# Kernel tuning notes

Hardware: AMD Instinct MI355X
Metric: run time of the kernel (lower is better)

Reference implementation:

```python
import jax, jax.numpy as jnp
import numpy as np

B, T, E = 8, 2048, 512  # batch, seq_len, dim (single head, head_dim == dim)
EPS = 1e-3


def setup_inputs() -> dict:
    key = jax.random.key(0)
    ks = jax.random.split(key, 6)
    s = E ** -0.5  # scale proj weights like nn.Linear init so exp(k) stays finite
    return {
        "x": jax.random.normal(ks[0], (B, E, T), jnp.float32),
        "toep_weight": jax.random.normal(ks[1], (1, T), jnp.float32),
        "q_w": jax.random.normal(ks[2], (E, E), jnp.float32) * s,
        "q_b": jnp.zeros((E,), jnp.float32),
        "k_w": jax.random.normal(ks[3], (E, E), jnp.float32) * s,
        "k_b": jnp.zeros((E,), jnp.float32),
        "v_w": jax.random.normal(ks[4], (E, E), jnp.float32) * s,
        "v_b": jnp.zeros((E,), jnp.float32),
        "o_w": jax.random.normal(ks[5], (E, E), jnp.float32) * s,
        "o_b": jnp.zeros((E,), jnp.float32),
    }


def reference(x, toep_weight, q_w, q_b, k_w, k_b, v_w, v_b, o_w, o_b):
    # x: (B, E, T) -> (B, T, E)
    xt = jnp.transpose(x, (0, 2, 1))
    q = xt @ q_w.T + q_b
    k = xt @ k_w.T + k_b
    v = xt @ v_w.T + v_b
    # feature maps: softmax(q) * d^-1/2 , exp(k); v scaled by per-position Toeplitz weight
    q = jax.nn.softmax(q, axis=-1) * (E ** -0.5)
    k = jnp.exp(k)
    v = v * toep_weight[0][:, None]  # (T,1) broadcast over (B,T,E)
    # causal linear attention: running outer-product state S (B,E,E) and key-sum z (B,E)
    qs = jnp.transpose(q, (1, 0, 2))  # (T, B, E)
    kk = jnp.transpose(k, (1, 0, 2))
    vv = jnp.transpose(v, (1, 0, 2))

    def step(carry, inp):
        S, z = carry
        qt, kt, vt = inp  # each (B, E)
        S = S + kt[:, :, None] * vt[:, None, :]  # cumulative k v^T
        z = z + kt                                # cumulative key sum
        d = jnp.maximum(jnp.sum(z * qt, axis=-1), EPS)  # clamp then reciprocal
        out = jnp.einsum('bd,bde->be', qt, S) / d[:, None]
        return (S, z), out

    S0 = jnp.zeros((B, E, E), q.dtype)
    z0 = jnp.zeros((B, E), q.dtype)
    _, outs = jax.lax.scan(step, (S0, z0), (qs, kk, vv))  # outs: (T, B, E)
    attn = jnp.transpose(outs, (1, 0, 2))  # (B, T, E)
    return attn @ o_w.T + o_b
```

## Files before the change

### kernel.cpp

```cpp
#include <hip/hip_runtime.h>
#include <hip/hip_bf16.h>
#include <math.h>
#include <stdint.h>

#define B_ 8
#define T_ 2048
#define E_ 512
#define CCH 256
#define NC_ 8
#define EPS_ 1e-3f
#define QSCALE 0.044194173824159216f

typedef __attribute__((ext_vector_type(8))) short short8;
typedef __attribute__((ext_vector_type(4))) float f32x4;
typedef __hip_bfloat16 bf16_t;

__device__ __forceinline__ short f2bs(float x) {
    bf16_t h = __float2bfloat16(x);
    return __builtin_bit_cast(short, h);
}

__device__ __forceinline__ void async16(const void* g, void* l) {
    __builtin_amdgcn_global_load_lds(
        (const __attribute__((address_space(1))) unsigned int*)(unsigned long long)(uintptr_t)g,
        (__attribute__((address_space(3))) unsigned int*)(unsigned int)(uintptr_t)l,
        16, 0, 0);
}

__device__ __forceinline__ void gemm128(const short* __restrict__ Ag, int lda,
                                        const short* __restrict__ Bg, int ldb, int K,
                                        short* Al, short* Bl, f32x4 acc[4][4],
                                        int wm, int wn, int wq, int lane) {
    int m16 = lane & 15, quad = lane >> 4;
    for (int k0 = 0; k0 < K; k0 += 32) {
        __syncthreads();
        #pragma unroll
        for (int cc = 0; cc < 2; ++cc) {
            int row = wq * 32 + cc * 16 + (lane >> 2);
            int kc = (lane & 3) * 8;
            async16(Ag + (size_t)row * lda + k0 + kc, Al + (wq * 32 + cc * 16) * 32);
            async16(Bg + (size_t)row * ldb + k0 + kc, Bl + (wq * 32 + cc * 16) * 32);
        }
        __syncthreads();
        short8 a[4], b[4];
        #pragma unroll
        for (int i = 0; i < 4; ++i)
            a[i] = *(const short8*)(Al + (wm + i * 16 + m16) * 32 + quad * 8);
        #pragma unroll
        for (int i = 0; i < 4; ++i)
            b[i] = *(const short8*)(Bl + (wn + i * 16 + m16) * 32 + quad * 8);
        #pragma unroll
        for (int i = 0; i < 4; ++i)
            #pragma unroll
            for (int j = 0; j < 4; ++j)
                acc[i][j] = __builtin_amdgcn_mfma_f32_16x16x32_bf16(a[i], b[j], acc[i][j], 0, 0, 0);
    }
}

#define GEMM_PROLOG \
    int tid = threadIdx.x, lane = tid & 63, wq = tid >> 6; \
    int wm = (wq & 1) * 64, wn = (wq >> 1) * 64; \
    int m16 = lane & 15, quad = lane >> 4; \
    (void)tid; \
    f32x4 acc[4][4]; \
    { f32x4 zz = {0.f, 0.f, 0.f, 0.f}; \
      for (int i = 0; i < 4; ++i) for (int j = 0; j < 4; ++j) acc[i][j] = zz; }

__global__ void castw_kernel(const float* __restrict__ qw, const float* __restrict__ kw,
                             const float* __restrict__ vw, const float* __restrict__ ow,
                             short* __restrict__ wbf) {
    size_t idx8 = ((size_t)blockIdx.x * 256 + threadIdx.x) * 8;
    int sel = (int)(idx8 >> 18);
    size_t off = idx8 & ((1u << 18) - 1);
    const float* src = sel == 0 ? qw : sel == 1 ? kw : sel == 2 ? vw : ow;
    const float4* sp = (const float4*)(src + off);
    float4 a = sp[0], b = sp[1];
    short8 g;
    g[0] = f2bs(a.x); g[1] = f2bs(a.y); g[2] = f2bs(a.z); g[3] = f2bs(a.w);
    g[4] = f2bs(b.x); g[5] = f2bs(b.y); g[6] = f2bs(b.z); g[7] = f2bs(b.w);
    *(short8*)(wbf + idx8) = g;
}

__global__ void transpose_x_kernel(const float* __restrict__ x, short* __restrict__ xbf) {
    __shared__ __align__(16) float S[64][68];
    int tid = threadIdx.x;
    int t0 = blockIdx.x * 64, e0 = blockIdx.y * 64, b = blockIdx.z;
    const float* src = x + ((size_t)b * E_ + e0) * T_ + t0;
    short* dst = xbf + ((size_t)b * T_ + t0) * E_ + e0;
    #pragma unroll
    for (int p = 0; p < 2; ++p) {
        int el = p * 32 + (tid >> 3), tc = (tid & 7) * 8;
        const float4* sp = (const float4*)(src + (size_t)el * T_ + tc);
        *(float4*)&S[el][tc] = sp[0];
        *(float4*)&S[el][tc + 4] = sp[1];
    }
    __syncthreads();
    #pragma unroll
    for (int p = 0; p < 2; ++p) {
        int tl = p * 32 + (tid >> 3), ec = (tid & 7) * 8;
        short8 g;
        #pragma unroll
        for (int j = 0; j < 8; ++j) g[j] = f2bs(S[ec + j][tl]);
        *(short8*)(dst + (size_t)tl * E_ + ec) = g;
    }
}

__global__ void transpose_bf_kernel(const short* __restrict__ k, const short* __restrict__ v,
                                    short* __restrict__ kT, short* __restrict__ vT) {
    __shared__ __align__(16) short S[64][72];
    int tid = threadIdx.x;
    int t0 = blockIdx.x * 64, e0 = blockIdx.y * 64;
    int b = blockIdx.z >> 1, which = blockIdx.z & 1;
    const short* src = (which ? v : k) + ((size_t)b * T_ + t0) * E_ + e0;
    short* dst = (which ? vT : kT) + ((size_t)b * E_ + e0) * T_ + t0;
    #pragma unroll
    for (int p = 0; p < 2; ++p) {
        int tl = p * 32 + (tid >> 3), ec = (tid & 7) * 8;
        *(short8*)&S[tl][ec] = *(const short8*)(src + (size_t)tl * E_ + ec);
    }
    __syncthreads();
    #pragma unroll
    for (int p = 0; p < 2; ++p) {
        int er = p * 32 + (tid >> 3), tc = (tid & 7) * 8;
        short8 g;
        #pragma unroll
        for (int j = 0; j < 8; ++j) g[j] = S[tc + j][er];
        *(short8*)(dst + (size_t)er * T_ + tc) = g;
    }
}

__global__ __launch_bounds__(256) void proj_qkv_kernel(
    const short* __restrict__ xbf, const short* __restrict__ wbf,
    const float* __restrict__ qb, const float* __restrict__ kb, const float* __restrict__ vb,
    const float* __restrict__ toep,
    float* __restrict__ qf, bf16_t* __restrict__ kout, bf16_t* __restrict__ vout) {
    __shared__ __align__(16) short Al[128 * 32], Bl[128 * 32];
    GEMM_PROLOG
    int t0 = blockIdx.x * 128, i0 = blockIdx.y * 128;
    int b = blockIdx.z / 3, sel = blockIdx.z % 3;
    const short* Ag = xbf + ((size_t)b * T_ + t0) * E_;
    const short* Bg = wbf + (size_t)sel * E_ * E_ + (size_t)i0 * E_;
    gemm128(Ag, E_, Bg, E_, E_, Al, Bl, acc, wm, wn, wq, lane);
    const float* bias = (sel == 0) ? qb : (sel == 1) ? kb : vb;
    #pragma unroll
    for (int mt = 0; mt < 4; ++mt)
        #pragma unroll
        for (int r = 0; r < 4; ++r) {
            int t = t0 + wm + mt * 16 + quad * 4 + r;
            size_t rowoff = ((size_t)b * T_ + t) * E_;
            float tw = toep[t];
            #pragma unroll
            for (int nt = 0; nt < 4; ++nt) {
                int col = i0 + wn + nt * 16 + m16;
                float vv = acc[mt][nt][r] + bias[col];
                if (sel == 0) qf[rowoff + col] = vv;
                else if (sel == 1) kout[rowoff + col] = __float2bfloat16(expf(vv));
                else vout[rowoff + col] = __float2bfloat16(vv * tw);
            }
        }
}

__global__ void softmax_kernel(const float* __restrict__ qf, bf16_t* __restrict__ qbf) {
    __shared__ float red[256];
    int row = blockIdx.x, tid = threadIdx.x;
    const float* p = qf + (size_t)row * E_;
    float v0 = p[tid], v1 = p[tid + 256];
    red[tid] = fmaxf(v0, v1);
    __syncthreads();
    for (int s = 128; s > 0; s >>= 1) { if (tid < s) red[tid] = fmaxf(red[tid], red[tid + s]); __syncthreads(); }
    float m = red[0];
    __syncthreads();
    float e0 = expf(v0 - m), e1 = expf(v1 - m);
    red[tid] = e0 + e1;
    __syncthreads();
    for (int s = 128; s > 0; s >>= 1) { if (tid < s) red[tid] += red[tid + s]; __syncthreads(); }
    float inv = QSCALE / red[0];
    qbf[(size_t)row * E_ + tid] = __float2bfloat16(e0 * inv);
    qbf[(size_t)row * E_ + tid + 256] = __float2bfloat16(e1 * inv);
}

__global__ __launch_bounds__(256) void chunk_kv_kernel(
    const short* __restrict__ vT, const short* __restrict__ kT, bf16_t* __restrict__ KV) {
    __shared__ __align__(16) short Al[128 * 32], Bl[128 * 32];
    GEMM_PROLOG
    int ev0 = blockIdx.x * 128, ek0 = blockIdx.y * 128;
    int bc = blockIdx.z, b = bc >> 3, c = bc & 7;
    const short* Ag = vT + ((size_t)b * E_ + ev0) * T_ + c * CCH;
    const short* Bg = kT + ((size_t)b * E_ + ek0) * T_ + c * CCH;
    gemm128(Ag, T_, Bg, T_, CCH, Al, Bl, acc, wm, wn, wq, lane);
    #pragma unroll
    for (int mt = 0; mt < 4; ++mt)
        #pragma unroll
        for (int r = 0; r < 4; ++r) {
            int ev = ev0 + wm + mt * 16 + quad * 4 + r;
            #pragma unroll
            for (int nt = 0; nt < 4; ++nt) {
                int ek = ek0 + wn + nt * 16 + m16;
                KV[((size_t)bc * E_ + ev) * E_ + ek] = __float2bfloat16(acc[mt][nt][r]);
            }
        }
}

__global__ void scan_kv_kernel(bf16_t* __restrict__ KV) {
    size_t gid = (size_t)blockIdx.x * 256 + threadIdx.x;
    size_t b = gid >> 18, idx = gid & ((1u << 18) - 1);
    bf16_t* p = KV + b * ((size_t)NC_ * E_ * E_) + idx;
    float run = 0.f;
    for (int c = 0; c < NC_; ++c) {
        float t = __bfloat162float(*p);
        *p = __float2bfloat16(run);
        run += t;
        p += (size_t)E_ * E_;
    }
}

__global__ void ksum_kernel(const bf16_t* __restrict__ k, float* __restrict__ ks) {
    int bc = blockIdx.x, b = bc >> 3, c = bc & 7;
    int e = blockIdx.y * 256 + threadIdx.x;
    const bf16_t* kp = k + ((size_t)b * T_ + (size_t)c * CCH) * E_ + e;
    float s = 0.f;
    for (int t = 0; t < CCH; ++t) s += __bfloat162float(kp[(size_t)t * E_]);
    ks[(size_t)bc * E_ + e] = s;
}
__global__ void scan_f_kernel(float* __restrict__ buf, int nper) {
    int gid = blockIdx.x * 256 + threadIdx.x;
    int b = gid / nper, idx = gid % nper;
    float run = 0.f;
    float* p = buf + (size_t)b * NC_ * nper + idx;
    for (int c = 0; c < NC_; ++c) { float t = *p; *p = run; run += t; p += nper; }
}

__global__ __launch_bounds__(256) void pmat_kernel(
    const short* __restrict__ qbf, const short* __restrict__ kbf, bf16_t* __restrict__ P) {
    __shared__ __align__(16) short Al[128 * 32], Bl[128 * 32];
    int tj0 = blockIdx.x * 128, ti0 = blockIdx.y * 128;
    int bc = blockIdx.z, b = bc >> 3, c = bc & 7;
    short* Pp = (short*)P + (size_t)bc * CCH * CCH;
    if (tj0 > ti0) {
        short8 z8 = {0, 0, 0, 0, 0, 0, 0, 0};
        for (int i = threadIdx.x; i < 128 * 128 / 8; i += 256) {
            int row = i >> 4, colc = (i * 8) & 127;
            *(short8*)(Pp + (size_t)(ti0 + row) * CCH + tj0 + colc) = z8;
        }
        return;
    }
    GEMM_PROLOG
    const short* Ag = qbf + ((size_t)b * T_ + c * CCH + ti0) * E_;
    const short* Bg = kbf + ((size_t)b * T_ + c * CCH + tj0) * E_;
    gemm128(Ag, E_, Bg, E_, E_, Al, Bl, acc, wm, wn, wq, lane);
    #pragma unroll
    for (int mt = 0; mt < 4; ++mt)
        #pragma unroll
        for (int r = 0; r < 4; ++r) {
            int row = ti0 + wm + mt * 16 + quad * 4 + r;
            #pragma unroll
            for (int nt = 0; nt < 4; ++nt) {
                int col = tj0 + wn + nt * 16 + m16;
                float vv = (col <= row) ? acc[mt][nt][r] : 0.f;
                ((bf16_t*)Pp)[(size_t)row * CCH + col] = __float2bfloat16(vv);
            }
        }
}

__global__ void denom_kernel(const bf16_t* __restrict__ qbf, const float* __restrict__ z,
                             const bf16_t* __restrict__ P, float* __restrict__ invd) {
    __shared__ float red[256];
    int row = blockIdx.x, tid = threadIdx.x;
    int b = row >> 11, t = row & (T_ - 1);
    int c = t >> 8, tl = t & 255;
    const bf16_t* qr = qbf + (size_t)row * E_;
    const float* zr = z + ((size_t)(b * NC_ + c)) * E_;
    const bf16_t* Pr = P + (((size_t)(b * NC_ + c)) * CCH + tl) * CCH;
    float s = __bfloat162float(qr[tid]) * zr[tid]
            + __bfloat162float(qr[tid + 256]) * zr[tid + 256]
            + __bfloat162float(Pr[tid]);
    red[tid] = s;
    __syncthreads();
    for (int st = 128; st > 0; st >>= 1) { if (tid < st) red[tid] += red[tid + st]; __syncthreads(); }
    if (tid == 0) invd[row] = 1.f / fmaxf(red[0], EPS_);
}

__global__ __launch_bounds__(256) void attnout_kernel(
    const short* __restrict__ qbf, const short* __restrict__ KV,
    const short* __restrict__ P, const short* __restrict__ vT,
    const float* __restrict__ invd, bf16_t* __restrict__ attn) {
    __shared__ __align__(16) short Al[128 * 32], Bl[128 * 32];
    GEMM_PROLOG
    int t0 = blockIdx.x * 128, i0 = blockIdx.y * 128, b = blockIdx.z;
    int c = t0 >> 8, tl0 = t0 & 255, bc = b * NC_ + c;
    gemm128(qbf + ((size_t)b * T_ + t0) * E_, E_,
            KV + ((size_t)bc * E_ + i0) * E_, E_, E_, Al, Bl, acc, wm, wn, wq, lane);
    gemm128(P + ((size_t)bc * CCH + tl0) * CCH, CCH,
            vT + ((size_t)b * E_ + i0) * T_ + c * CCH, T_, CCH, Al, Bl, acc, wm, wn, wq, lane);
    #pragma unroll
    for (int mt = 0; mt < 4; ++mt)
        #pragma unroll
        for (int r = 0; r < 4; ++r) {
            int t = t0 + wm + mt * 16 + quad * 4 + r;
            float sc = invd[(size_t)b * T_ + t];
            #pragma unroll
            for (int nt = 0; nt < 4; ++nt) {
                int col = i0 + wn + nt * 16 + m16;
                attn[((size_t)b * T_ + t) * E_ + col] = __float2bfloat16(acc[mt][nt][r] * sc);
            }
        }
}

__global__ __launch_bounds__(256) void outproj_kernel(
    const short* __restrict__ attn, const short* __restrict__ wbf_o,
    const float* __restrict__ ob, float* __restrict__ out) {
    __shared__ __align__(16) short Al[128 * 32], Bl[128 * 32];
    GEMM_PROLOG
    int t0 = blockIdx.x * 128, i0 = blockIdx.y * 128, b = blockIdx.z;
    gemm128(attn + ((size_t)b * T_ + t0) * E_, E_,
            wbf_o + (size_t)i0 * E_, E_, E_, Al, Bl, acc, wm, wn, wq, lane);
    #pragma unroll
    for (int mt = 0; mt < 4; ++mt)
        #pragma unroll
        for (int r = 0; r < 4; ++r) {
            int t = t0 + wm + mt * 16 + quad * 4 + r;
            #pragma unroll
            for (int nt = 0; nt < 4; ++nt) {
                int col = i0 + wn + nt * 16 + m16;
                out[((size_t)b * T_ + t) * E_ + col] = acc[mt][nt][r] + ob[col];
            }
        }
}

extern "C" void kernel_launch(void* const* d_in, const int* in_sizes, int n_in,
                              void* d_out, int out_size, void* d_ws, size_t ws_size,
                              hipStream_t stream) {
    const float* x    = (const float*)d_in[0];
    const float* toep = (const float*)d_in[1];
    const float* q_w  = (const float*)d_in[2];
    const float* q_b  = (const float*)d_in[3];
    const float* k_w  = (const float*)d_in[4];
    const float* k_b  = (const float*)d_in[5];
    const float* v_w  = (const float*)d_in[6];
    const float* v_b  = (const float*)d_in[7];
    const float* o_w  = (const float*)d_in[8];
    const float* o_b  = (const float*)d_in[9];

    const size_t NTE = (size_t)B_ * T_ * E_;
    char* base = (char*)d_ws;
    short* xbf  = (short*)base;  base += NTE * 2;
    short* wbf  = (short*)base;  base += (size_t)4 * E_ * E_ * 2;
    short* qbf  = (short*)base;  base += NTE * 2;
    short* kbf  = (short*)base;  base += NTE * 2;
    short* vbf  = (short*)base;  base += NTE * 2;
    short* kT   = (short*)base;  base += NTE * 2;
    short* vT   = (short*)base;  base += NTE * 2;
    short* KV   = (short*)base;  base += (size_t)B_ * NC_ * E_ * E_ * 2;
    short* P    = (short*)base;  base += (size_t)B_ * NC_ * CCH * CCH * 2;
    float* ksum = (float*)base;  base += (size_t)B_ * NC_ * E_ * 4;
    float* invd = (float*)base;  base += (size_t)B_ * T_ * 4;
    float* qf   = (float*)base;  base += NTE * 4;
    short* attn = xbf;
    float* out  = (float*)d_out;

    dim3 blk(256);
    castw_kernel<<<dim3(512), blk, 0, stream>>>(q_w, k_w, v_w, o_w, wbf);
    transpose_x_kernel<<<dim3(32, 8, 8), blk, 0, stream>>>(x, xbf);
    proj_qkv_kernel<<<dim3(16, 4, 24), blk, 0, stream>>>(
        xbf, wbf, q_b, k_b, v_b, toep, qf, (bf16_t*)kbf, (bf16_t*)vbf);
    softmax_kernel<<<dim3(B_ * T_), blk, 0, stream>>>(qf, (bf16_t*)qbf);
    transpose_bf_kernel<<<dim3(32, 8, 16), blk, 0, stream>>>(kbf, vbf, kT, vT);
    chunk_kv_kernel<<<dim3(4, 4, 64), blk, 0, stream>>>(vT, kT, (bf16_t*)KV);
    scan_kv_kernel<<<dim3(8192), blk, 0, stream>>>((bf16_t*)KV);
    ksum_kernel<<<dim3(64, 2), blk, 0, stream>>>((const bf16_t*)kbf, ksum);
    scan_f_kernel<<<dim3(16), blk, 0, stream>>>(ksum, E_);
    pmat_kernel<<<dim3(2, 2, 64), blk, 0, stream>>>(qbf, kbf, (bf16_t*)P);
    denom_kernel<<<dim3(B_ * T_), blk, 0, stream>>>(
        (const bf16_t*)qbf, ksum, (const bf16_t*)P, invd);
    attnout_kernel<<<dim3(16, 4, 8), blk, 0, stream>>>(
        qbf, KV, P, vT, invd, (bf16_t*)attn);
    outproj_kernel<<<dim3(16, 4, 8), blk, 0, stream>>>(
        attn, wbf + (size_t)3 * E_ * E_, o_b, out);
}
```

Before: 296.4 us.

## Double GEMM K-step to 64 with swizzled LDS layout; store raw q as bf16

The shared GEMM helper now stages 64-wide K tiles per barrier pair instead of 32. The LDS layout is rearranged so each async 16-byte load covers 8 rows by 64 columns, and the MFMA operand reads follow that layout. This halves the number of synchronisations per GEMM at the cost of twice the LDS per block. Separately, the pre-softmax q projection is written as bf16 instead of fp32, which halves that intermediate's traffic but adds rounding error before the softmax.

```diff
diff --git a/kernel.cpp b/kernel.cpp
--- a/kernel.cpp
+++ b/kernel.cpp
@@ -32,28 +32,32 @@
                                         short* Al, short* Bl, f32x4 acc[4][4],
                                         int wm, int wn, int wq, int lane) {
     int m16 = lane & 15, quad = lane >> 4;
-    for (int k0 = 0; k0 < K; k0 += 32) {
+    int r8 = lane & 7, c8 = (lane >> 3) * 8;
+    for (int k0 = 0; k0 < K; k0 += 64) {
         __syncthreads();
         #pragma unroll
-        for (int cc = 0; cc < 2; ++cc) {
-            int row = wq * 32 + cc * 16 + (lane >> 2);
-            int kc = (lane & 3) * 8;
-            async16(Ag + (size_t)row * lda + k0 + kc, Al + (wq * 32 + cc * 16) * 32);
-            async16(Bg + (size_t)row * ldb + k0 + kc, Bl + (wq * 32 + cc * 16) * 32);
+        for (int w = 0; w < 4; ++w) {
+            int R = wq * 32 + w * 8;
+            async16(Ag + (size_t)(R + r8) * lda + k0 + c8, Al + R * 64);
+            async16(Bg + (size_t)(R + r8) * ldb + k0 + c8, Bl + R * 64);
         }
         __syncthreads();
-        short8 a[4], b[4];
-        #pragma unroll
-        for (int i = 0; i < 4; ++i)
-            a[i] = *(const short8*)(Al + (wm + i * 16 + m16) * 32 + quad * 8);
-        #pragma unroll
-        for (int i = 0; i < 4; ++i)
-            b[i] = *(const short8*)(Bl + (wn + i * 16 + m16) * 32 + quad * 8);
-        #pragma unroll
-        for (int i = 0; i < 4; ++i)
-            #pragma unroll
-            for (int j = 0; j < 4; ++j)
-                acc[i][j] = __builtin_amdgcn_mfma_f32_16x16x32_bf16(a[i], b[j], acc[i][j], 0, 0, 0);
+        #pragma unroll
+        for (int h = 0; h < 2; ++h) {
+            int co = (h * 4 + quad) * 64 + (m16 >> 3) * 512 + (m16 & 7) * 8;
+            short8 a[4], b[4];
+            #pragma unroll
+            for (int i = 0; i < 4; ++i)
+                a[i] = *(const short8*)(Al + (wm + i * 16) * 64 + co);
+            #pragma unroll
+            for (int i = 0; i < 4; ++i)
+                b[i] = *(const short8*)(Bl + (wn + i * 16) * 64 + co);
+            #pragma unroll
+            for (int i = 0; i < 4; ++i)
+                #pragma unroll
+                for (int j = 0; j < 4; ++j)
+                    acc[i][j] = __builtin_amdgcn_mfma_f32_16x16x32_bf16(a[i], b[j], acc[i][j], 0, 0, 0);
+        }
     }
 }
 
@@ -133,8 +137,8 @@
     const short* __restrict__ xbf, const short* __restrict__ wbf,
     const float* __restrict__ qb, const float* __restrict__ kb, const float* __restrict__ vb,
     const float* __restrict__ toep,
-    float* __restrict__ qf, bf16_t* __restrict__ kout, bf16_t* __restrict__ vout) {
-    __shared__ __align__(16) short Al[128 * 32], Bl[128 * 32];
+    bf16_t* __restrict__ qraw, bf16_t* __restrict__ kout, bf16_t* __restrict__ vout) {
+    __shared__ __align__(16) short Al[128 * 64], Bl[128 * 64];
     GEMM_PROLOG
     int t0 = blockIdx.x * 128, i0 = blockIdx.y * 128;
     int b = blockIdx.z / 3, sel = blockIdx.z % 3;
@@ -153,18 +157,18 @@
             for (int nt = 0; nt < 4; ++nt) {
                 int col = i0 + wn + nt * 16 + m16;
                 float vv = acc[mt][nt][r] + bias[col];
-                if (sel == 0) qf[rowoff + col] = vv;
+                if (sel == 0) qraw[rowoff + col] = __float2bfloat16(vv);
                 else if (sel == 1) kout[rowoff + col] = __float2bfloat16(expf(vv));
                 else vout[rowoff + col] = __float2bfloat16(vv * tw);
             }
         }
 }
 
-__global__ void softmax_kernel(const float* __restrict__ qf, bf16_t* __restrict__ qbf) {
+__global__ void softmax_kernel(const bf16_t* __restrict__ qraw, bf16_t* __restrict__ qbf) {
     __shared__ float red[256];
     int row = blockIdx.x, tid = threadIdx.x;
-    const float* p = qf + (size_t)row * E_;
-    float v0 = p[tid], v1 = p[tid + 256];
+    const bf16_t* p = qraw + (size_t)row * E_;
+    float v0 = __bfloat162float(p[tid]), v1 = __bfloat162float(p[tid + 256]);
     red[tid] = fmaxf(v0, v1);
     __syncthreads();
     for (int s = 128; s > 0; s >>= 1) { if (tid < s) red[tid] = fmaxf(red[tid], red[tid + s]); __syncthreads(); }
@@ -181,7 +185,7 @@
 
 __global__ __launch_bounds__(256) void chunk_kv_kernel(
     const short* __restrict__ vT, const short* __restrict__ kT, bf16_t* __restrict__ KV) {
-    __shared__ __align__(16) short Al[128 * 32], Bl[128 * 32];
+    __shared__ __align__(16) short Al[128 * 64], Bl[128 * 64];
     GEMM_PROLOG
     int ev0 = blockIdx.x * 128, ek0 = blockIdx.y * 128;
     int bc = blockIdx.z, b = bc >> 3, c = bc & 7;
@@ -232,7 +236,7 @@
 
 __global__ __launch_bounds__(256) void pmat_kernel(
     const short* __restrict__ qbf, const short* __restrict__ kbf, bf16_t* __restrict__ P) {
-    __shared__ __align__(16) short Al[128 * 32], Bl[128 * 32];
+    __shared__ __align__(16) short Al[128 * 64], Bl[128 * 64];
     int tj0 = blockIdx.x * 128, ti0 = blockIdx.y * 128;
     int bc = blockIdx.z, b = bc >> 3, c = bc & 7;
     short* Pp = (short*)P + (size_t)bc * CCH * CCH;
@@ -284,7 +288,7 @@
     const short* __restrict__ qbf, const short* __restrict__ KV,
     const short* __restrict__ P, const short* __restrict__ vT,
     const float* __restrict__ invd, bf16_t* __restrict__ attn) {
-    __shared__ __align__(16) short Al[128 * 32], Bl[128 * 32];
+    __shared__ __align__(16) short Al[128 * 64], Bl[128 * 64];
     GEMM_PROLOG
     int t0 = blockIdx.x * 128, i0 = blockIdx.y * 128, b = blockIdx.z;
     int c = t0 >> 8, tl0 = t0 & 255, bc = b * NC_ + c;
@@ -309,7 +313,7 @@
 __global__ __launch_bounds__(256) void outproj_kernel(
     const short* __restrict__ attn, const short* __restrict__ wbf_o,
     const float* __restrict__ ob, float* __restrict__ out) {
-    __shared__ __align__(16) short Al[128 * 32], Bl[128 * 32];
+    __shared__ __align__(16) short Al[128 * 64], Bl[128 * 64];
     GEMM_PROLOG
     int t0 = blockIdx.x * 128, i0 = blockIdx.y * 128, b = blockIdx.z;
     gemm128(attn + ((size_t)b * T_ + t0) * E_, E_,
@@ -345,6 +349,7 @@
     char* base = (char*)d_ws;
     short* xbf  = (short*)base;  base += NTE * 2;
     short* wbf  = (short*)base;  base += (size_t)4 * E_ * E_ * 2;
+    short* qraw = (short*)base;  base += NTE * 2;
     short* qbf  = (short*)base;  base += NTE * 2;
     short* kbf  = (short*)base;  base += NTE * 2;
     short* vbf  = (short*)base;  base += NTE * 2;
@@ -354,7 +359,6 @@
     short* P    = (short*)base;  base += (size_t)B_ * NC_ * CCH * CCH * 2;
     float* ksum = (float*)base;  base += (size_t)B_ * NC_ * E_ * 4;
     float* invd = (float*)base;  base += (size_t)B_ * T_ * 4;
-    float* qf   = (float*)base;  base += NTE * 4;
     short* attn = xbf;
     float* out  = (float*)d_out;
 
@@ -362,8 +366,8 @@
     castw_kernel<<<dim3(512), blk, 0, stream>>>(q_w, k_w, v_w, o_w, wbf);
     transpose_x_kernel<<<dim3(32, 8, 8), blk, 0, stream>>>(x, xbf);
     proj_qkv_kernel<<<dim3(16, 4, 24), blk, 0, stream>>>(
-        xbf, wbf, q_b, k_b, v_b, toep, qf, (bf16_t*)kbf, (bf16_t*)vbf);
-    softmax_kernel<<<dim3(B_ * T_), blk, 0, stream>>>(qf, (bf16_t*)qbf);
+        xbf, wbf, q_b, k_b, v_b, toep, (bf16_t*)qraw, (bf16_t*)kbf, (bf16_t*)vbf);
+    softmax_kernel<<<dim3(B_ * T_), blk, 0, stream>>>((const bf16_t*)qraw, (bf16_t*)qbf);
     transpose_bf_kernel<<<dim3(32, 8, 16), blk, 0, stream>>>(kbf, vbf, kT, vT);
     chunk_kv_kernel<<<dim3(4, 4, 64), blk, 0, stream>>>(vT, kT, (bf16_t*)KV);
     scan_kv_kernel<<<dim3(8192), blk, 0, stream>>>((bf16_t*)KV);
```

New measurement: 319.8 us. +7.9%, slower.

## Merge independent launches, store q as bf16, and rework LDS layout in GEMM

Applied to the files above, without the earlier changes.

Independent kernels are merged into combined launches that branch on block index: weight cast with x transpose, softmax with key-sum, chunk KV with P matrix, and the two prefix scans. This cuts the kernel count from 12 to 8 and lets small kernels share the GPU with larger ones. The raw q projection is now written as bf16 instead of fp32, halving that intermediate's traffic at the cost of rounding before softmax. The async LDS load layout in gemm128 is changed so each wave fills contiguous 16-row windows and fragments are read with a different stride, likely to reduce bank conflicts.

```diff
diff --git a/kernel.cpp b/kernel.cpp
--- a/kernel.cpp
+++ b/kernel.cpp
@@ -32,23 +32,24 @@
                                         short* Al, short* Bl, f32x4 acc[4][4],
                                         int wm, int wn, int wq, int lane) {
     int m16 = lane & 15, quad = lane >> 4;
+    int r16 = lane & 15, c4 = (lane >> 4) * 8;
     for (int k0 = 0; k0 < K; k0 += 32) {
         __syncthreads();
         #pragma unroll
-        for (int cc = 0; cc < 2; ++cc) {
-            int row = wq * 32 + cc * 16 + (lane >> 2);
-            int kc = (lane & 3) * 8;
-            async16(Ag + (size_t)row * lda + k0 + kc, Al + (wq * 32 + cc * 16) * 32);
-            async16(Bg + (size_t)row * ldb + k0 + kc, Bl + (wq * 32 + cc * 16) * 32);
+        for (int w = 0; w < 2; ++w) {
+            int win = wq + w * 4;
+            int R = win * 16;
+            async16(Ag + (size_t)(R + r16) * lda + k0 + c4, Al + win * 512);
+            async16(Bg + (size_t)(R + r16) * ldb + k0 + c4, Bl + win * 512);
         }
         __syncthreads();
         short8 a[4], b[4];
         #pragma unroll
         for (int i = 0; i < 4; ++i)
-            a[i] = *(const short8*)(Al + (wm + i * 16 + m16) * 32 + quad * 8);
+            a[i] = *(const short8*)(Al + (wm + i * 16) * 32 + quad * 128 + m16 * 8);
         #pragma unroll
         for (int i = 0; i < 4; ++i)
-            b[i] = *(const short8*)(Bl + (wn + i * 16 + m16) * 32 + quad * 8);
+            b[i] = *(const short8*)(Bl + (wn + i * 16) * 32 + quad * 128 + m16 * 8);
         #pragma unroll
         for (int i = 0; i < 4; ++i)
             #pragma unroll
@@ -66,25 +67,28 @@
     { f32x4 zz = {0.f, 0.f, 0.f, 0.f}; \
       for (int i = 0; i < 4; ++i) for (int j = 0; j < 4; ++j) acc[i][j] = zz; }
 
-__global__ void castw_kernel(const float* __restrict__ qw, const float* __restrict__ kw,
-                             const float* __restrict__ vw, const float* __restrict__ ow,
-                             short* __restrict__ wbf) {
-    size_t idx8 = ((size_t)blockIdx.x * 256 + threadIdx.x) * 8;
-    int sel = (int)(idx8 >> 18);
-    size_t off = idx8 & ((1u << 18) - 1);
-    const float* src = sel == 0 ? qw : sel == 1 ? kw : sel == 2 ? vw : ow;
-    const float4* sp = (const float4*)(src + off);
-    float4 a = sp[0], b = sp[1];
-    short8 g;
-    g[0] = f2bs(a.x); g[1] = f2bs(a.y); g[2] = f2bs(a.z); g[3] = f2bs(a.w);
-    g[4] = f2bs(b.x); g[5] = f2bs(b.y); g[6] = f2bs(b.z); g[7] = f2bs(b.w);
-    *(short8*)(wbf + idx8) = g;
-}
-
-__global__ void transpose_x_kernel(const float* __restrict__ x, short* __restrict__ xbf) {
+__global__ void prep_kernel(const float* __restrict__ qw, const float* __restrict__ kw,
+                            const float* __restrict__ vw, const float* __restrict__ ow,
+                            short* __restrict__ wbf,
+                            const float* __restrict__ x, short* __restrict__ xbf) {
+    int bid = blockIdx.x;
+    int tid = threadIdx.x;
+    if (bid < 512) {
+        size_t idx8 = ((size_t)bid * 256 + tid) * 8;
+        int sel = (int)(idx8 >> 18);
+        size_t off = idx8 & ((1u << 18) - 1);
+        const float* src = sel == 0 ? qw : sel == 1 ? kw : sel == 2 ? vw : ow;
+        const float4* sp = (const float4*)(src + off);
+        float4 a = sp[0], b = sp[1];
+        short8 g;
+        g[0] = f2bs(a.x); g[1] = f2bs(a.y); g[2] = f2bs(a.z); g[3] = f2bs(a.w);
+        g[4] = f2bs(b.x); g[5] = f2bs(b.y); g[6] = f2bs(b.z); g[7] = f2bs(b.w);
+        *(short8*)(wbf + idx8) = g;
+        return;
+    }
+    bid -= 512;
     __shared__ __align__(16) float S[64][68];
-    int tid = threadIdx.x;
-    int t0 = blockIdx.x * 64, e0 = blockIdx.y * 64, b = blockIdx.z;
+    int t0 = (bid & 31) * 64, e0 = ((bid >> 5) & 7) * 64, b = bid >> 8;
     const float* src = x + ((size_t)b * E_ + e0) * T_ + t0;
     short* dst = xbf + ((size_t)b * T_ + t0) * E_ + e0;
     #pragma unroll
@@ -133,7 +137,7 @@
     const short* __restrict__ xbf, const short* __restrict__ wbf,
     const float* __restrict__ qb, const float* __restrict__ kb, const float* __restrict__ vb,
     const float* __restrict__ toep,
-    float* __restrict__ qf, bf16_t* __restrict__ kout, bf16_t* __restrict__ vout) {
+    bf16_t* __restrict__ qraw, bf16_t* __restrict__ kout, bf16_t* __restrict__ vout) {
     __shared__ __align__(16) short Al[128 * 32], Bl[128 * 32];
     GEMM_PROLOG
     int t0 = blockIdx.x * 128, i0 = blockIdx.y * 128;
@@ -153,18 +157,29 @@
             for (int nt = 0; nt < 4; ++nt) {
                 int col = i0 + wn + nt * 16 + m16;
                 float vv = acc[mt][nt][r] + bias[col];
-                if (sel == 0) qf[rowoff + col] = vv;
+                if (sel == 0) qraw[rowoff + col] = __float2bfloat16(vv);
                 else if (sel == 1) kout[rowoff + col] = __float2bfloat16(expf(vv));
                 else vout[rowoff + col] = __float2bfloat16(vv * tw);
             }
         }
 }
 
-__global__ void softmax_kernel(const float* __restrict__ qf, bf16_t* __restrict__ qbf) {
+__global__ void softmax_ksum_kernel(const bf16_t* __restrict__ qraw, bf16_t* __restrict__ qbf,
+                                    const bf16_t* __restrict__ k, float* __restrict__ ks) {
+    int bid = blockIdx.x, tid = threadIdx.x;
+    if (bid >= B_ * T_) {
+        int r = bid - B_ * T_;
+        int bc = r >> 1, b = bc >> 3, c = bc & 7;
+        int e = (r & 1) * 256 + tid;
+        const bf16_t* kp = k + ((size_t)b * T_ + (size_t)c * CCH) * E_ + e;
+        float s = 0.f;
+        for (int t = 0; t < CCH; ++t) s += __bfloat162float(kp[(size_t)t * E_]);
+        ks[(size_t)bc * E_ + e] = s;
+        return;
+    }
     __shared__ float red[256];
-    int row = blockIdx.x, tid = threadIdx.x;
-    const float* p = qf + (size_t)row * E_;
-    float v0 = p[tid], v1 = p[tid + 256];
+    const bf16_t* p = qraw + (size_t)bid * E_;
+    float v0 = __bfloat162float(p[tid]), v1 = __bfloat162float(p[tid + 256]);
     red[tid] = fmaxf(v0, v1);
     __syncthreads();
     for (int s = 128; s > 0; s >>= 1) { if (tid < s) red[tid] = fmaxf(red[tid], red[tid + s]); __syncthreads(); }
@@ -175,66 +190,38 @@
     __syncthreads();
     for (int s = 128; s > 0; s >>= 1) { if (tid < s) red[tid] += red[tid + s]; __syncthreads(); }
     float inv = QSCALE / red[0];
-    qbf[(size_t)row * E_ + tid] = __float2bfloat16(e0 * inv);
-    qbf[(size_t)row * E_ + tid + 256] = __float2bfloat16(e1 * inv);
-}
-
-__global__ __launch_bounds__(256) void chunk_kv_kernel(
-    const short* __restrict__ vT, const short* __restrict__ kT, bf16_t* __restrict__ KV) {
-    __shared__ __align__(16) short Al[128 * 32], Bl[128 * 32];
-    GEMM_PROLOG
-    int ev0 = blockIdx.x * 128, ek0 = blockIdx.y * 128;
-    int bc = blockIdx.z, b = bc >> 3, c = bc & 7;
-    const short* Ag = vT + ((size_t)b * E_ + ev0) * T_ + c * CCH;
-    const short* Bg = kT + ((size_t)b * E_ + ek0) * T_ + c * CCH;
-    gemm128(Ag, T_, Bg, T_, CCH, Al, Bl, acc, wm, wn, wq, lane);
-    #pragma unroll
-    for (int mt = 0; mt < 4; ++mt)
-        #pragma unroll
-        for (int r = 0; r < 4; ++r) {
-            int ev = ev0 + wm + mt * 16 + quad * 4 + r;
-            #pragma unroll
-            for (int nt = 0; nt < 4; ++nt) {
-                int ek = ek0 + wn + nt * 16 + m16;
-                KV[((size_t)bc * E_ + ev) * E_ + ek] = __float2bfloat16(acc[mt][nt][r]);
-            }
-        }
-}
-
-__global__ void scan_kv_kernel(bf16_t* __restrict__ KV) {
-    size_t gid = (size_t)blockIdx.x * 256 + threadIdx.x;
-    size_t b = gid >> 18, idx = gid & ((1u << 18) - 1);
-    bf16_t* p = KV + b * ((size_t)NC_ * E_ * E_) + idx;
-    float run = 0.f;
-    for (int c = 0; c < NC_; ++c) {
-        float t = __bfloat162float(*p);
-        *p = __float2bfloat16(run);
-        run += t;
-        p += (size_t)E_ * E_;
-    }
-}
-
-__global__ void ksum_kernel(const bf16_t* __restrict__ k, float* __restrict__ ks) {
-    int bc = blockIdx.x, b = bc >> 3, c = bc & 7;
-    int e = blockIdx.y * 256 + threadIdx.x;
-    const bf16_t* kp = k + ((size_t)b * T_ + (size_t)c * CCH) * E_ + e;
-    float s = 0.f;
-    for (int t = 0; t < CCH; ++t) s += __bfloat162float(kp[(size_t)t * E_]);
-    ks[(size_t)bc * E_ + e] = s;
-}
-__global__ void scan_f_kernel(float* __restrict__ buf, int nper) {
-    int gid = blockIdx.x * 256 + threadIdx.x;
-    int b = gid / nper, idx = gid % nper;
-    float run = 0.f;
-    float* p = buf + (size_t)b * NC_ * nper + idx;
-    for (int c = 0; c < NC_; ++c) { float t = *p; *p = run; run += t; p += nper; }
-}
-
-__global__ __launch_bounds__(256) void pmat_kernel(
+    qbf[(size_t)bid * E_ + tid] = __float2bfloat16(e0 * inv);
+    qbf[(size_t)bid * E_ + tid + 256] = __float2bfloat16(e1 * inv);
+}
+
+__global__ __launch_bounds__(256) void kvp_kernel(
+    const short* __restrict__ vT, const short* __restrict__ kT, bf16_t* __restrict__ KV,
     const short* __restrict__ qbf, const short* __restrict__ kbf, bf16_t* __restrict__ P) {
     __shared__ __align__(16) short Al[128 * 32], Bl[128 * 32];
-    int tj0 = blockIdx.x * 128, ti0 = blockIdx.y * 128;
-    int bc = blockIdx.z, b = bc >> 3, c = bc & 7;
+    int bid = blockIdx.x;
+    if (bid < 1024) {
+        GEMM_PROLOG
+        int ev0 = (bid & 3) * 128, ek0 = ((bid >> 2) & 3) * 128;
+        int bc = bid >> 4, b = bc >> 3, c = bc & 7;
+        const short* Ag = vT + ((size_t)b * E_ + ev0) * T_ + c * CCH;
+        const short* Bg = kT + ((size_t)b * E_ + ek0) * T_ + c * CCH;
+        gemm128(Ag, T_, Bg, T_, CCH, Al, Bl, acc, wm, wn, wq, lane);
+        #pragma unroll
+        for (int mt = 0; mt < 4; ++mt)
+            #pragma unroll
+            for (int r = 0; r < 4; ++r) {
+                int ev = ev0 + wm + mt * 16 + quad * 4 + r;
+                #pragma unroll
+                for (int nt = 0; nt < 4; ++nt) {
+                    int ek = ek0 + wn + nt * 16 + m16;
+                    KV[((size_t)bc * E_ + ev) * E_ + ek] = __float2bfloat16(acc[mt][nt][r]);
+                }
+            }
+        return;
+    }
+    bid -= 1024;
+    int tj0 = (bid & 1) * 128, ti0 = ((bid >> 1) & 1) * 128;
+    int bc = bid >> 2, b = bc >> 3, c = bc & 7;
     short* Pp = (short*)P + (size_t)bc * CCH * CCH;
     if (tj0 > ti0) {
         short8 z8 = {0, 0, 0, 0, 0, 0, 0, 0};
@@ -260,6 +247,28 @@
                 ((bf16_t*)Pp)[(size_t)row * CCH + col] = __float2bfloat16(vv);
             }
         }
+}
+
+__global__ void scan2_kernel(bf16_t* __restrict__ KV, float* __restrict__ ks) {
+    size_t bid = blockIdx.x;
+    if (bid < 8192) {
+        size_t gid = bid * 256 + threadIdx.x;
+        size_t b = gid >> 18, idx = gid & ((1u << 18) - 1);
+        bf16_t* p = KV + b * ((size_t)NC_ * E_ * E_) + idx;
+        float run = 0.f;
+        for (int c = 0; c < NC_; ++c) {
+            float t = __bfloat162float(*p);
+            *p = __float2bfloat16(run);
+            run += t;
+            p += (size_t)E_ * E_;
+        }
+        return;
+    }
+    int gid = (int)(bid - 8192) * 256 + threadIdx.x;
+    int b = gid >> 9, idx = gid & (E_ - 1);
+    float run = 0.f;
+    float* p = ks + (size_t)b * NC_ * E_ + idx;
+    for (int c = 0; c < NC_; ++c) { float t = *p; *p = run; run += t; p += E_; }
 }
 
 __global__ void denom_kernel(const bf16_t* __restrict__ qbf, const float* __restrict__ z,
@@ -345,6 +354,7 @@
     char* base = (char*)d_ws;
     short* xbf  = (short*)base;  base += NTE * 2;
     short* wbf  = (short*)base;  base += (size_t)4 * E_ * E_ * 2;
+    short* qraw = (short*)base;  base += NTE * 2;
     short* qbf  = (short*)base;  base += NTE * 2;
     short* kbf  = (short*)base;  base += NTE * 2;
     short* vbf  = (short*)base;  base += NTE * 2;
@@ -354,22 +364,19 @@
     short* P    = (short*)base;  base += (size_t)B_ * NC_ * CCH * CCH * 2;
     float* ksum = (float*)base;  base += (size_t)B_ * NC_ * E_ * 4;
     float* invd = (float*)base;  base += (size_t)B_ * T_ * 4;
-    float* qf   = (float*)base;  base += NTE * 4;
     short* attn = xbf;
     float* out  = (float*)d_out;
 
     dim3 blk(256);
-    castw_kernel<<<dim3(512), blk, 0, stream>>>(q_w, k_w, v_w, o_w, wbf);
-    transpose_x_kernel<<<dim3(32, 8, 8), blk, 0, stream>>>(x, xbf);
+    prep_kernel<<<dim3(2560), blk, 0, stream>>>(q_w, k_w, v_w, o_w, wbf, x, xbf);
     proj_qkv_kernel<<<dim3(16, 4, 24), blk, 0, stream>>>(
-        xbf, wbf, q_b, k_b, v_b, toep, qf, (bf16_t*)kbf, (bf16_t*)vbf);
-    softmax_kernel<<<dim3(B_ * T_), blk, 0, stream>>>(qf, (bf16_t*)qbf);
+        xbf, wbf, q_b, k_b, v_b, toep, (bf16_t*)qraw, (bf16_t*)kbf, (bf16_t*)vbf);
+    softmax_ksum_kernel<<<dim3(B_ * T_ + 128), blk, 0, stream>>>(
+        (const bf16_t*)qraw, (bf16_t*)qbf, (const bf16_t*)kbf, ksum);
     transpose_bf_kernel<<<dim3(32, 8, 16), blk, 0, stream>>>(kbf, vbf, kT, vT);
-    chunk_kv_kernel<<<dim3(4, 4, 64), blk, 0, stream>>>(vT, kT, (bf16_t*)KV);
-    scan_kv_kernel<<<dim3(8192), blk, 0, stream>>>((bf16_t*)KV);
-    ksum_kernel<<<dim3(64, 2), blk, 0, stream>>>((const bf16_t*)kbf, ksum);
-    scan_f_kernel<<<dim3(16), blk, 0, stream>>>(ksum, E_);
-    pmat_kernel<<<dim3(2, 2, 64), blk, 0, stream>>>(qbf, kbf, (bf16_t*)P);
+    kvp_kernel<<<dim3(1280), blk, 0, stream>>>(
+        vT, kT, (bf16_t*)KV, qbf, kbf, (bf16_t*)P);
+    scan2_kernel<<<dim3(8208), blk, 0, stream>>>((bf16_t*)KV, ksum);
     denom_kernel<<<dim3(B_ * T_), blk, 0, stream>>>(
         (const bf16_t*)qbf, ksum, (const bf16_t*)P, invd);
     attnout_kernel<<<dim3(16, 4, 8), blk, 0, stream>>>(
```

Result: slower. 310.9 us (+4.9%).
